# Kernel tuning notes

Measured on AMD Instinct MI355X. Metric: run time of the kernel, lower is better.

## Reference

```python
import jax, jax.numpy as jnp
import numpy as np

B, S, E, D, M, HN, NH, T, NS, OUT = 64, 196, 512, 2048, 25, 32, 8, 50, 512, 1000
HD = E // NH


def setup_inputs() -> dict:
    key = jax.random.key(0)
    ks = jax.random.split(key, 24)
    rn = lambda k, sh, sc: jax.random.normal(k, sh, jnp.float32) * sc
    iv = lambda n: 1.0 / np.sqrt(n).astype(np.float32)
    inp = {}
    inp['x'] = rn(ks[0], (B, S, E), 1.0)
    inp['Wkv'] = rn(ks[1], (E, E), iv(E)); inp['bkv'] = jnp.zeros((E,))
    inp['g_kv'] = jnp.ones((E,)); inp['b_kv'] = jnp.zeros((E,))
    inp['Wq'] = rn(ks[2], (NS, E), iv(NS)); inp['bq'] = jnp.zeros((E,))
    inp['Wqa'] = rn(ks[3], (E, E), iv(E)); inp['bqa'] = jnp.zeros((E,))
    inp['Wka'] = rn(ks[4], (E, E), iv(E)); inp['bka'] = jnp.zeros((E,))
    inp['Wva'] = rn(ks[5], (E, E), iv(E)); inp['bva'] = jnp.zeros((E,))
    inp['Wo'] = rn(ks[6], (E, E), iv(E)); inp['bo'] = jnp.zeros((E,))
    inp['Wsyn'] = rn(ks[7], (E + D, 2 * D), iv(E + D)); inp['bsyn'] = jnp.zeros((2 * D,))
    inp['g_syn'] = jnp.ones((D,)); inp['b_syn'] = jnp.zeros((D,))
    inp['w1'] = rn(ks[8], (M, 2 * HN, D), iv(M)); inp['b1'] = jnp.zeros((D, 2 * HN))
    inp['w2'] = rn(ks[9], (HN, 2, D), iv(HN)); inp['b2'] = jnp.zeros((D, 2))
    inp['start_act'] = rn(ks[10], (D,), iv(D))
    inp['start_trace'] = rn(ks[11], (D, M), iv(D + M))
    inp['decay_action'] = jax.random.uniform(ks[12], (NS,), jnp.float32)
    inp['decay_out'] = jax.random.uniform(ks[13], (NS,), jnp.float32)
    inp['Wout'] = rn(ks[14], (NS, OUT), iv(NS)); inp['bout'] = jnp.zeros((OUT,))
    inp['idx_act_l'] = jax.random.randint(ks[15], (NS,), 0, D, jnp.int32)
    inp['idx_act_r'] = jax.random.randint(ks[16], (NS,), 0, D, jnp.int32)
    inp['idx_out_l'] = jax.random.randint(ks[17], (NS,), 0, D, jnp.int32)
    inp['idx_out_r'] = jax.random.randint(ks[18], (NS,), 0, D, jnp.int32)
    return inp


def _ln(v, g, b):
    mu = v.mean(-1, keepdims=True)
    var = ((v - mu) ** 2).mean(-1, keepdims=True)
    return (v - mu) / jnp.sqrt(var + 1e-5) * g + b


def _glu(v):
    h = v.shape[-1] // 2
    return v[..., :h] * jax.nn.sigmoid(v[..., h:])


def reference(x, Wkv, bkv, g_kv, b_kv, Wq, bq, Wqa, bqa, Wka, bka, Wva, bva, Wo, bo,
              Wsyn, bsyn, g_syn, b_syn, w1, b1, w2, b2, start_act, start_trace,
              decay_action, decay_out, Wout, bout,
              idx_act_l, idx_act_r, idx_out_l, idx_out_r):
    # kv features: LazyLinear + LayerNorm (backbone='none')
    kv = _ln(x @ Wkv + bkv, g_kv, b_kv)                      # (B,S,E)
    kh = (kv @ Wka + bka).reshape(B, S, NH, HD)               # precompute K/V heads
    vh = (kv @ Wva + bva).reshape(B, S, NH, HD)
    rA = jnp.exp(-jnp.clip(decay_action, 0.0, 15.0))[None]    # (1,NS)
    rO = jnp.exp(-jnp.clip(decay_out, 0.0, 15.0))[None]
    act0 = jnp.broadcast_to(start_act[None], (B, D))
    tr0 = jnp.broadcast_to(start_trace[None], (B, D, M))
    # initial 'out' sync from start state (decay_alpha=None branch)
    aO0 = act0[:, idx_out_l] * act0[:, idx_out_r]
    bO0 = jnp.ones_like(aO0)
    aA0 = jnp.zeros((B, NS), x.dtype)
    bA0 = jnp.zeros((B, NS), x.dtype)

    def nlm(tr):  # private per-neuron deep MLPs over memory history
        h = _glu(jnp.einsum('bdm,mhd->bdh', tr, w1) + b1[None])
        o = _glu(jnp.einsum('bdh,hod->bdo', h, w2) + b2[None])
        return o[..., 0]                                      # (B,D)

    def step(carry, _):
        tr, act, aA, bA, aO, bO = carry
        pA = act[:, idx_act_l] * act[:, idx_act_r]
        aA = rA * aA + pA
        bA = rA * bA + 1.0
        syncA = aA / jnp.sqrt(bA)
        q = syncA @ Wq + bq                                   # (B,E)
        qh = (q @ Wqa + bqa).reshape(B, NH, HD)
        sc = jnp.einsum('bhd,bshd->bhs', qh, kh) / np.sqrt(HD).astype(np.float32)
        attn = jnp.einsum('bhs,bshd->bhd', jax.nn.softmax(sc, -1), vh)
        attn = attn.reshape(B, E) @ Wo + bo
        pre = jnp.concatenate([attn, act], -1)                # (B,E+D)
        s = _ln(_glu(pre @ Wsyn + bsyn), g_syn, b_syn)        # synapse MLP -> (B,D)
        tr = jnp.concatenate([tr[:, :, 1:], s[:, :, None]], -1)
        act = nlm(tr)
        pO = act[:, idx_out_l] * act[:, idx_out_r]
        aO = rO * aO + pO
        bO = rO * bO + 1.0
        syncO = aO / jnp.sqrt(bO)
        pred = syncO @ Wout + bout                            # (B,OUT)
        logp = jax.nn.log_softmax(pred, -1)
        ne = -(jnp.exp(logp) * logp).sum(-1) / np.log(OUT).astype(np.float32)
        cert = jnp.stack([ne, 1.0 - ne], -1)                  # (B,2)
        return (tr, act, aA, bA, aO, bO), (pred, cert)

    carry, (preds, certs) = jax.lax.scan(step, (tr0, act0, aA0, bA0, aO0, bO0), None, length=T)
    predictions = jnp.moveaxis(preds, 0, -1)                  # (B,OUT,T)
    certainties = jnp.moveaxis(certs, 0, -1)                  # (B,2,T)
    sync_out_final = carry[4] / jnp.sqrt(carry[5])
    return predictions, certainties, sync_out_final
```

## Files before the change

kernel.cpp:

```cpp
#include <hip/hip_runtime.h>

#define BB 64
#define SS 196
#define EE 512
#define DD 2048
#define MM 25
#define HNN 32
#define NHH 8
#define TT 50
#define NSS 512
#define OUTN 1000
#define HDD 64
#define KSYN 2560
#define NSYN 4096

#define CERT_OFF 3200000
#define SYNC_OFF 3206400

__device__ __forceinline__ float sigm(float x){ return 1.f / (1.f + expf(-x)); }
__device__ __forceinline__ int rfl(int x){ return __builtin_amdgcn_readfirstlane(x); }

template<int LAYOUT>
__global__ __launch_bounds__(256) void sgemm(
    const float* __restrict__ Ag, const float* __restrict__ Wg,
    const float* __restrict__ bias, float* __restrict__ Cg,
    int Mg, int Ng, int Kg, int ro)
{
  __shared__ float As[16][68];
  __shared__ float Bs[16][68];
  int t = threadIdx.x;
  int bm = blockIdx.x * 64, bn = blockIdx.y * 64;
  int ty = t >> 4, tx = t & 15;
  int atm = t >> 2, atk = (t & 3) * 4;
  int bkk = t >> 4, bnn = (t & 15) * 4;
  float c[4][4] = {};
  for (int k0 = 0; k0 < Kg; k0 += 16){
    float4 av = *reinterpret_cast<const float4*>(Ag + (size_t)(bm + atm) * Kg + k0 + atk);
    As[atk][atm] = av.x; As[atk + 1][atm] = av.y;
    As[atk + 2][atm] = av.z; As[atk + 3][atm] = av.w;
    float4 bv = *reinterpret_cast<const float4*>(Wg + (size_t)(k0 + bkk) * Ng + bn + bnn);
    *reinterpret_cast<float4*>(&Bs[bkk][bnn]) = bv;
    __syncthreads();
    #pragma unroll
    for (int k = 0; k < 16; k++){
      float4 a = *reinterpret_cast<const float4*>(&As[k][ty * 4]);
      float4 b = *reinterpret_cast<const float4*>(&Bs[k][tx * 4]);
      c[0][0] += a.x * b.x; c[0][1] += a.x * b.y; c[0][2] += a.x * b.z; c[0][3] += a.x * b.w;
      c[1][0] += a.y * b.x; c[1][1] += a.y * b.y; c[1][2] += a.y * b.z; c[1][3] += a.y * b.w;
      c[2][0] += a.z * b.x; c[2][1] += a.z * b.y; c[2][2] += a.z * b.z; c[2][3] += a.z * b.w;
      c[3][0] += a.w * b.x; c[3][1] += a.w * b.y; c[3][2] += a.w * b.z; c[3][3] += a.w * b.w;
    }
    __syncthreads();
  }
  #pragma unroll
  for (int j = 0; j < 4; j++){
    int col = bn + tx * 4 + j;
    float bvv = bias ? bias[col] : 0.f;
    #pragma unroll
    for (int i = 0; i < 4; i++){
      int row = bm + ty * 4 + i;
      float v = c[i][j] + bvv;
      if (LAYOUT == 0){
        Cg[(size_t)row * Ng + col] = v;
      } else {
        int tok = ro + row;
        int b = tok / SS, s = tok - b * SS;
        int h = col >> 6, dh = col & 63;
        if (LAYOUT == 1) Cg[(((size_t)b * NHH + h) * SS + s) * HDD + dh] = v;
        else             Cg[(((size_t)b * NHH + h) * HDD + dh) * SS + s] = v;
      }
    }
  }
}

__global__ __launch_bounds__(256) void ln_rows_kernel(const float* __restrict__ y,
    const float* __restrict__ g, const float* __restrict__ bb,
    float* __restrict__ outf)
{
  int r = blockIdx.x, t = threadIdx.x;
  __shared__ float red[256];
  const float* row = y + (size_t)r * EE;
  float v0 = row[t], v1 = row[t + 256];
  red[t] = v0 + v1; __syncthreads();
  for (int st = 128; st > 0; st >>= 1){ if (t < st) red[t] += red[t + st]; __syncthreads(); }
  float mean = red[0] * (1.f / EE); __syncthreads();
  float d0 = v0 - mean, d1 = v1 - mean;
  red[t] = d0 * d0 + d1 * d1; __syncthreads();
  for (int st = 128; st > 0; st >>= 1){ if (t < st) red[t] += red[t + st]; __syncthreads(); }
  float rs = 1.f / sqrtf(red[0] * (1.f / EE) + 1e-5f);
  float* orow = outf + (size_t)r * EE;
  orow[t] = d0 * rs * g[t] + bb[t];
  orow[t + 256] = d1 * rs * g[t + 256] + bb[t + 256];
}

__global__ __launch_bounds__(512) void bqq_kernel(const float* __restrict__ bq,
    const float* __restrict__ Wqa, const float* __restrict__ bqa, float* __restrict__ bqq)
{
  __shared__ float s[EE];
  int t = threadIdx.x;
  s[t] = bq[t]; __syncthreads();
  float a0 = 0, a1 = 0, a2 = 0, a3 = 0;
  #pragma unroll 8
  for (int k = 0; k < EE; k += 4){
    a0 += s[k]     * Wqa[(size_t)(k)     * EE + t];
    a1 += s[k + 1] * Wqa[(size_t)(k + 1) * EE + t];
    a2 += s[k + 2] * Wqa[(size_t)(k + 2) * EE + t];
    a3 += s[k + 3] * Wqa[(size_t)(k + 3) * EE + t];
  }
  bqq[t] = bqa[t] + ((a0 + a1) + (a2 + a3));
}

__global__ __launch_bounds__(512) void prep_decay(const float* __restrict__ dcA,
    const float* __restrict__ dcO, float* __restrict__ rA, float* __restrict__ rO)
{
  int t = threadIdx.x;
  rA[t] = expf(-fminf(fmaxf(dcA[t], 0.f), 15.f));
  rO[t] = expf(-fminf(fmaxf(dcO[t], 0.f), 15.f));
}

__global__ __launch_bounds__(256) void permute_wsyn(const float* __restrict__ Wsyn,
    float* __restrict__ W2)
{
  int k = blockIdx.x;
  const float* src = Wsyn + (size_t)k * NSYN;
  float* dst = W2 + (size_t)k * NSYN;
  for (int c = threadIdx.x; c < 2048; c += 256){
    float2 v; v.x = src[c]; v.y = src[2048 + c];
    *reinterpret_cast<float2*>(&dst[2 * c]) = v;
  }
}

__global__ __launch_bounds__(256) void init_kernel(const float* __restrict__ sa,
    const float* __restrict__ strace,
    const int* __restrict__ ol, const int* __restrict__ orr,
    float* __restrict__ act, float* __restrict__ tr,
    float* __restrict__ aA, float* __restrict__ bA,
    float* __restrict__ aO, float* __restrict__ bO,
    float* __restrict__ psum, float* __restrict__ psq)
{
  int tid = blockIdx.x * 256 + threadIdx.x;
  if (tid < 128){ psum[tid] = 0.f; psq[tid] = 0.f; }
  int b = tid >> 11, d = tid & 2047;
  act[(size_t)d * 64 + b] = sa[d];
  for (int m = 0; m < MM; m++)
    tr[((size_t)m * DD + d) * 64 + b] = strace[d * MM + m];
  if (tid < BB * NSS){
    int n = tid & (NSS - 1);
    int b2 = tid >> 9;
    aO[(size_t)b2 * NSS + n] = sa[ol[n]] * sa[orr[n]];
    bO[(size_t)b2 * NSS + n] = 1.f;
    aA[(size_t)b2 * NSS + n] = 0.f;
    bA[(size_t)b2 * NSS + n] = 0.f;
  }
}

__global__ __launch_bounds__(512) void k_front(
    const float* __restrict__ khT, const float* __restrict__ vh,
    const float* __restrict__ Wqq, const float* __restrict__ bqq,
    const float* __restrict__ Wo, const float* __restrict__ bo,
    const float* __restrict__ rA, const float* __restrict__ rO,
    const int* __restrict__ ial, const int* __restrict__ iar,
    const int* __restrict__ iol, const int* __restrict__ ior,
    float* __restrict__ aA, float* __restrict__ bA,
    float* __restrict__ aO, float* __restrict__ bO,
    const float* __restrict__ act, float* __restrict__ A,
    float* __restrict__ so_g, float* __restrict__ dout, int t)
{
  __shared__ float sm[4096];
  const int tid = threadIdx.x, b = blockIdx.x;
  const int lane = tid & 63, wv = tid >> 6;
  {
    int n = tid;
    if (t < TT){
      float pa = act[(size_t)ial[n] * 64 + b] * act[(size_t)iar[n] * 64 + b];
      float r = rA[n];
      float na = r * aA[(size_t)b * NSS + n] + pa;
      float nb = r * bA[(size_t)b * NSS + n] + 1.f;
      aA[(size_t)b * NSS + n] = na; bA[(size_t)b * NSS + n] = nb;
      sm[n] = na / sqrtf(nb);
    }
    if (t > 0){
      float po = act[(size_t)iol[n] * 64 + b] * act[(size_t)ior[n] * 64 + b];
      float r2 = rO[n];
      float na2 = r2 * aO[(size_t)b * NSS + n] + po;
      float nb2 = r2 * bO[(size_t)b * NSS + n] + 1.f;
      aO[(size_t)b * NSS + n] = na2; bO[(size_t)b * NSS + n] = nb2;
      float sv = na2 / sqrtf(nb2);
      so_g[(size_t)b * NSS + n] = sv;
      if (t == TT) dout[SYNC_OFF + (size_t)b * NSS + n] = sv;
    }
  }
  if (t >= TT) return;
  __syncthreads();
  {
    int e = tid;
    float a0 = 0, a1 = 0, a2 = 0, a3 = 0;
    #pragma unroll 8
    for (int k = 0; k < EE; k += 4){
      a0 += sm[k]     * Wqq[(size_t)(k)     * EE + e];
      a1 += sm[k + 1] * Wqq[(size_t)(k + 1) * EE + e];
      a2 += sm[k + 2] * Wqq[(size_t)(k + 2) * EE + e];
      a3 += sm[k + 3] * Wqq[(size_t)(k + 3) * EE + e];
    }
    sm[1024 + e] = bqq[e] + ((a0 + a1) + (a2 + a3));
  }
  __syncthreads();
  {
    int h = wv;
    int u = b * NHH + h;
    const float* K = khT + (size_t)u * HDD * SS;
    const float* V = vh + (size_t)u * SS * HDD;
    float c0 = 0, c1 = 0, c2 = 0, c3 = 0;
    for (int d2 = 0; d2 < HDD; d2++){
      float qd = sm[1024 + h * 64 + d2];
      const float* Kr = K + (size_t)d2 * SS;
      c0 += qd * Kr[lane];
      c1 += qd * Kr[64 + lane];
      c2 += qd * Kr[128 + lane];
      c3 += qd * Kr[192 + lane];
    }
    float s0 = c0 * 0.125f, s1 = c1 * 0.125f, s2 = c2 * 0.125f;
    float s3 = (lane < 4) ? c3 * 0.125f : -1e30f;
    float mx = fmaxf(fmaxf(s0, s1), fmaxf(s2, s3));
    #pragma unroll
    for (int off = 32; off > 0; off >>= 1)
      mx = fmaxf(mx, __shfl_xor(mx, off, 64));
    float e0 = expf(s0 - mx), e1 = expf(s1 - mx), e2 = expf(s2 - mx);
    float e3 = (lane < 4) ? expf(s3 - mx) : 0.f;
    float dn = e0 + e1 + e2 + e3;
    #pragma unroll
    for (int off = 32; off > 0; off >>= 1)
      dn += __shfl_xor(dn, off, 64);
    float* ps = sm + 1536 + h * 224;
    ps[lane] = e0; ps[64 + lane] = e1; ps[128 + lane] = e2;
    if (lane < 4) ps[192 + lane] = e3;
    float inv = 1.f / dn;
    float p0 = 0, p1 = 0, p2 = 0, p3 = 0;
    for (int s = 0; s < SS; s += 4){
      p0 += ps[s]     * V[(size_t)(s)     * 64 + lane];
      p1 += ps[s + 1] * V[(size_t)(s + 1) * 64 + lane];
      p2 += ps[s + 2] * V[(size_t)(s + 2) * 64 + lane];
      p3 += ps[s + 3] * V[(size_t)(s + 3) * 64 + lane];
    }
    sm[3328 + h * 64 + lane] = ((p0 + p1) + (p2 + p3)) * inv;
  }
  __syncthreads();
  {
    int e = tid;
    float a0 = 0, a1 = 0, a2 = 0, a3 = 0;
    #pragma unroll 8
    for (int k = 0; k < EE; k += 4){
      a0 += sm[3328 + k]     * Wo[(size_t)(k)     * EE + e];
      a1 += sm[3328 + k + 1] * Wo[(size_t)(k + 1) * EE + e];
      a2 += sm[3328 + k + 2] * Wo[(size_t)(k + 2) * EE + e];
      a3 += sm[3328 + k + 3] * Wo[(size_t)(k + 3) * EE + e];
    }
    A[(size_t)e * 64 + b] = bo[e] + ((a0 + a1) + (a2 + a3));
  }
}

__global__ __launch_bounds__(512) void k_syn2(
    const float* __restrict__ A, const float* __restrict__ W2,
    const float* __restrict__ bsyn, const float* __restrict__ Wout,
    const float* __restrict__ bout, const float* __restrict__ so_g,
    float* __restrict__ glupre, float* __restrict__ psum, float* __restrict__ psq,
    float* __restrict__ dout, int t)
{
  __shared__ float sm[8704];
  const int tid = threadIdx.x, blk = blockIdx.x;
  const int lane = tid & 63, wv = tid >> 6;
  const int par = t & 1;
  if (blk < 256){
    if (t >= TT) return;
    int c0 = blk * 8;
    int cc = 2 * c0;
    float acc[16];
    #pragma unroll
    for (int i = 0; i < 16; i++) acc[i] = 0.f;
    int kb = rfl(wv * 320);
    const float* Wp = W2 + (size_t)kb * NSYN + cc;
    const float* Ap = A + (size_t)kb * 64 + lane;
    for (int kt = 0; kt < 320; kt += 4){
      float a4[4];
      float4 w4[4][4];
      #pragma unroll
      for (int i = 0; i < 4; i++){
        a4[i] = Ap[(size_t)(kt + i) * 64];
        const float4* w = reinterpret_cast<const float4*>(Wp + (size_t)(kt + i) * NSYN);
        w4[i][0] = w[0]; w4[i][1] = w[1]; w4[i][2] = w[2]; w4[i][3] = w[3];
      }
      #pragma unroll
      for (int i = 0; i < 4; i++){
        float a = a4[i];
        acc[0]  += a * w4[i][0].x; acc[8]  += a * w4[i][0].y;
        acc[1]  += a * w4[i][0].z; acc[9]  += a * w4[i][0].w;
        acc[2]  += a * w4[i][1].x; acc[10] += a * w4[i][1].y;
        acc[3]  += a * w4[i][1].z; acc[11] += a * w4[i][1].w;
        acc[4]  += a * w4[i][2].x; acc[12] += a * w4[i][2].y;
        acc[5]  += a * w4[i][2].z; acc[13] += a * w4[i][2].w;
        acc[6]  += a * w4[i][3].x; acc[14] += a * w4[i][3].y;
        acc[7]  += a * w4[i][3].z; acc[15] += a * w4[i][3].w;
      }
    }
    #pragma unroll
    for (int i = 0; i < 16; i++) sm[wv * 1024 + i * 64 + lane] = acc[i];
    __syncthreads();
    {
      int ci = tid >> 6;
      int b = lane;
      float x0 = 0.f, x1 = 0.f;
      #pragma unroll
      for (int w = 0; w < 8; w++){
        x0 += sm[w * 1024 + ci * 64 + b];
        x1 += sm[w * 1024 + (8 + ci) * 64 + b];
      }
      x0 += bsyn[c0 + ci]; x1 += bsyn[2048 + c0 + ci];
      float u = x0 * sigm(x1);
      glupre[(size_t)(c0 + ci) * 64 + b] = u;
      sm[8192 + ci * 64 + b] = u;
    }
    __syncthreads();
    if (tid < 64){
      float s = 0.f, q = 0.f;
      #pragma unroll
      for (int c = 0; c < 8; c++){
        float uu = sm[8192 + c * 64 + tid];
        s += uu; q += uu * uu;
      }
      atomicAdd(&psum[par * 64 + tid], s);
      atomicAdd(&psq[par * 64 + tid], q);
    }
  } else {
    if (t == 0) return;
    int b = blk - 256;
    for (int k = tid; k < NSS; k += 512) sm[k] = so_g[(size_t)b * NSS + k];
    __syncthreads();
    #pragma unroll
    for (int half = 0; half < 2; half++){
      int n = tid + half * 512;
      if (n < OUTN){
        float a0 = 0, a1 = 0, a2 = 0, a3 = 0;
        #pragma unroll 8
        for (int k = 0; k < NSS; k += 4){
          a0 += sm[k]     * Wout[(size_t)(k)     * OUTN + n];
          a1 += sm[k + 1] * Wout[(size_t)(k + 1) * OUTN + n];
          a2 += sm[k + 2] * Wout[(size_t)(k + 2) * OUTN + n];
          a3 += sm[k + 3] * Wout[(size_t)(k + 3) * OUTN + n];
        }
        dout[((size_t)b * OUTN + n) * TT + (t - 1)] = bout[n] + ((a0 + a1) + (a2 + a3));
      }
    }
  }
}

__global__ __launch_bounds__(512) void k_nlm(
    const float* __restrict__ glupre, float* __restrict__ psum, float* __restrict__ psq,
    const float* __restrict__ gsyn, const float* __restrict__ bsn,
    const float* __restrict__ w1, const float* __restrict__ b1,
    const float* __restrict__ w2, const float* __restrict__ b2,
    float* __restrict__ tr, float* __restrict__ act, int t)
{
  __shared__ float sm[12800];
  const int tid = threadIdx.x, blk = blockIdx.x;
  const int lane = tid & 63, wv = tid >> 6;
  const int par = t & 1;
  if (blk == 0 && tid < 64){
    psum[(par ^ 1) * 64 + tid] = 0.f;
    psq[(par ^ 1) * 64 + tid] = 0.f;
  }
  int d0 = blk * 8;
  for (int idx = tid; idx < 1600; idx += 512){
    float4 va = *reinterpret_cast<const float4*>(w1 + (size_t)idx * DD + d0);
    float4 vb = *reinterpret_cast<const float4*>(w1 + (size_t)idx * DD + d0 + 4);
    sm[0 * 1600 + idx] = va.x; sm[1 * 1600 + idx] = va.y;
    sm[2 * 1600 + idx] = va.z; sm[3 * 1600 + idx] = va.w;
    sm[4 * 1600 + idx] = vb.x; sm[5 * 1600 + idx] = vb.y;
    sm[6 * 1600 + idx] = vb.z; sm[7 * 1600 + idx] = vb.w;
  }
  float ts = psum[par * 64 + lane];
  float tq = psq[par * 64 + lane];
  float mean = ts * (1.f / DD);
  float var = tq * (1.f / DD) - mean * mean;
  float rsv = 1.f / sqrtf(var + 1e-5f);
  __syncthreads();
  int dd = rfl(wv);
  int d = d0 + dd;
  float u = glupre[(size_t)d * 64 + lane];
  float snew = (u - mean) * rsv * gsyn[d] + bsn[d];
  int slot = t % MM;
  tr[((size_t)slot * DD + d) * 64 + lane] = snew;
  float hp[64];
  #pragma unroll
  for (int h = 0; h < 64; h++) hp[h] = b1[(size_t)d * 64 + h];
  for (int j = 0; j < MM - 1; j++){
    int js = (t + 1 + j) % MM;
    float tv = tr[((size_t)js * DD + d) * 64 + lane];
    const float* wr = &sm[dd * 1600 + j * 64];
    #pragma unroll
    for (int h4 = 0; h4 < 16; h4++){
      float4 w = *reinterpret_cast<const float4*>(&wr[h4 * 4]);
      hp[h4 * 4 + 0] += tv * w.x;
      hp[h4 * 4 + 1] += tv * w.y;
      hp[h4 * 4 + 2] += tv * w.z;
      hp[h4 * 4 + 3] += tv * w.w;
    }
  }
  {
    const float* wr = &sm[dd * 1600 + 24 * 64];
    #pragma unroll
    for (int h4 = 0; h4 < 16; h4++){
      float4 w = *reinterpret_cast<const float4*>(&wr[h4 * 4]);
      hp[h4 * 4 + 0] += snew * w.x;
      hp[h4 * 4 + 1] += snew * w.y;
      hp[h4 * 4 + 2] += snew * w.z;
      hp[h4 * 4 + 3] += snew * w.w;
    }
  }
  float o0 = b2[(size_t)d * 2], o1 = b2[(size_t)d * 2 + 1];
  #pragma unroll
  for (int h2 = 0; h2 < HNN; h2++){
    float hh = hp[h2] * sigm(hp[h2 + HNN]);
    o0 += hh * w2[((size_t)(h2 * 2)) * DD + d];
    o1 += hh * w2[((size_t)(h2 * 2 + 1)) * DD + d];
  }
  act[(size_t)d * 64 + lane] = o0 * sigm(o1);
}

__global__ __launch_bounds__(256) void cert_kernel(float* __restrict__ dout)
{
  int blk = blockIdx.x;
  int b = blk / TT, t = blk % TT;
  int tid = threadIdx.x;
  __shared__ float red[256];
  float vals[4];
  float mx = -1e30f;
  #pragma unroll
  for (int i = 0; i < 4; i++){
    int n = tid + i * 256;
    float v = (n < OUTN) ? dout[((size_t)b * OUTN + n) * TT + t] : -1e30f;
    vals[i] = v; mx = fmaxf(mx, v);
  }
  red[tid] = mx; __syncthreads();
  for (int st = 128; st > 0; st >>= 1){ if (tid < st) red[tid] = fmaxf(red[tid], red[tid + st]); __syncthreads(); }
  mx = red[0]; __syncthreads();
  float z = 0.f, s1 = 0.f;
  #pragma unroll
  for (int i = 0; i < 4; i++){
    int n = tid + i * 256;
    if (n < OUTN){
      float e = expf(vals[i] - mx);
      z += e; s1 += e * (vals[i] - mx);
    }
  }
  red[tid] = z; __syncthreads();
  for (int st = 128; st > 0; st >>= 1){ if (tid < st) red[tid] += red[tid + st]; __syncthreads(); }
  z = red[0]; __syncthreads();
  red[tid] = s1; __syncthreads();
  for (int st = 128; st > 0; st >>= 1){ if (tid < st) red[tid] += red[tid + st]; __syncthreads(); }
  s1 = red[0];
  if (tid == 0){
    float ne = (logf(z) - s1 / z) * (1.f / logf(1000.f));
    dout[CERT_OFF + ((size_t)b * 2 + 0) * TT + t] = ne;
    dout[CERT_OFF + ((size_t)b * 2 + 1) * TT + t] = 1.f - ne;
  }
}

extern "C" void kernel_launch(void* const* d_in, const int* in_sizes, int n_in,
                              void* d_out, int out_size, void* d_ws, size_t ws_size,
                              hipStream_t stream)
{
  const float* x    = (const float*)d_in[0];
  const float* Wkv  = (const float*)d_in[1];
  const float* bkv  = (const float*)d_in[2];
  const float* gkv  = (const float*)d_in[3];
  const float* bkv2 = (const float*)d_in[4];
  const float* Wq   = (const float*)d_in[5];
  const float* bq   = (const float*)d_in[6];
  const float* Wqa  = (const float*)d_in[7];
  const float* bqa  = (const float*)d_in[8];
  const float* Wka  = (const float*)d_in[9];
  const float* bka  = (const float*)d_in[10];
  const float* Wva  = (const float*)d_in[11];
  const float* bva  = (const float*)d_in[12];
  const float* Wo   = (const float*)d_in[13];
  const float* bo   = (const float*)d_in[14];
  const float* Wsyn = (const float*)d_in[15];
  const float* bsyn = (const float*)d_in[16];
  const float* gsyn = (const float*)d_in[17];
  const float* bsn  = (const float*)d_in[18];
  const float* w1   = (const float*)d_in[19];
  const float* b1   = (const float*)d_in[20];
  const float* w2   = (const float*)d_in[21];
  const float* b2   = (const float*)d_in[22];
  const float* sact = (const float*)d_in[23];
  const float* strc = (const float*)d_in[24];
  const float* dcA  = (const float*)d_in[25];
  const float* dcO  = (const float*)d_in[26];
  const float* Wout = (const float*)d_in[27];
  const float* bout = (const float*)d_in[28];
  const int* ial = (const int*)d_in[29];
  const int* iar = (const int*)d_in[30];
  const int* iol = (const int*)d_in[31];
  const int* ior = (const int*)d_in[32];

  char* ws = (char*)d_ws;
  float* khT  = (float*)(ws + 0);
  float* vh   = (float*)(ws + 25690112);
  float* B0   = (float*)(ws + 51380224);
  float* B1   = (float*)(ws + 64225280);
  float* tr    = (float*)(ws + 51380224);
  float* A     = (float*)(ws + 64487424);
  float* act   = A + 512 * 64;
  float* glupre= (float*)(ws + 65142784);
  float* aA    = (float*)(ws + 65667072);
  float* bA    = (float*)(ws + 65798144);
  float* aO    = (float*)(ws + 65929216);
  float* bO    = (float*)(ws + 66060288);
  float* so_g  = (float*)(ws + 66191360);
  float* Wqq   = (float*)(ws + 66322432);
  float* bqqb  = (float*)(ws + 67371008);
  float* rA    = (float*)(ws + 67373056);
  float* rO    = (float*)(ws + 67375104);
  float* psum  = (float*)(ws + 67377152);
  float* psq   = (float*)(ws + 67377664);
  float* W2    = (float*)(ws + 77070336);
  float* dout = (float*)d_out;

  for (int c = 0; c < 2; c++){
    const float* xc = x + (size_t)c * 6272 * EE;
    sgemm<0><<<dim3(98, 8), 256, 0, stream>>>(xc, Wkv, bkv, B0, 6272, EE, EE, 0);
    ln_rows_kernel<<<6272, 256, 0, stream>>>(B0, gkv, bkv2, B1);
    sgemm<3><<<dim3(98, 8), 256, 0, stream>>>(B1, Wka, bka, khT, 6272, EE, EE, c * 6272);
    sgemm<1><<<dim3(98, 8), 256, 0, stream>>>(B1, Wva, bva, vh, 6272, EE, EE, c * 6272);
  }
  sgemm<0><<<dim3(8, 8), 256, 0, stream>>>(Wq, Wqa, nullptr, Wqq, EE, EE, EE, 0);
  bqq_kernel<<<1, 512, 0, stream>>>(bq, Wqa, bqa, bqqb);
  permute_wsyn<<<KSYN, 256, 0, stream>>>(Wsyn, W2);
  prep_decay<<<1, 512, 0, stream>>>(dcA, dcO, rA, rO);
  init_kernel<<<512, 256, 0, stream>>>(sact, strc, iol, ior, act, tr, aA, bA, aO, bO,
                                       psum, psq);

  for (int t = 0; t < TT; t++){
    k_front<<<64, 512, 0, stream>>>(khT, vh, Wqq, bqqb, Wo, bo, rA, rO,
                                    ial, iar, iol, ior, aA, bA, aO, bO,
                                    act, A, so_g, dout, t);
    k_syn2<<<320, 512, 0, stream>>>(A, W2, bsyn, Wout, bout, so_g,
                                    glupre, psum, psq, dout, t);
    k_nlm<<<256, 512, 0, stream>>>(glupre, psum, psq, gsyn, bsn,
                                   w1, b1, w2, b2, tr, act, t);
  }
  k_front<<<64, 512, 0, stream>>>(khT, vh, Wqq, bqqb, Wo, bo, rA, rO,
                                  ial, iar, iol, ior, aA, bA, aO, bO,
                                  act, A, so_g, dout, TT);
  k_syn2<<<320, 512, 0, stream>>>(A, W2, bsyn, Wout, bout, so_g,
                                  glupre, psum, psq, dout, TT);
  cert_kernel<<<BB * TT, 256, 0, stream>>>(dout);
}
```

Baseline: 6.571 ms.

## Double k_front threads with split-K GEMVs and split attention heads

k_front now runs 1024 threads per block instead of 512. The two 512x512 GEMVs are split along K into two halves that are reduced through shared memory. Each attention head is handled by two waves, with cross-wave max and denominator reductions and split PV accumulation. This targets the latency of a kernel that launches only 64 blocks per step, at the cost of extra barriers and shared-memory reductions. Separately, the k_syn2 inner loop is unrolled to 8 rows per iteration to put more loads in flight, which raises register pressure.

```diff
diff --git a/kernel.cpp b/kernel.cpp
--- a/kernel.cpp
+++ b/kernel.cpp
@@ -154,7 +154,7 @@
   }
 }
 
-__global__ __launch_bounds__(512) void k_front(
+__global__ __launch_bounds__(1024) void k_front(
     const float* __restrict__ khT, const float* __restrict__ vh,
     const float* __restrict__ Wqq, const float* __restrict__ bqq,
     const float* __restrict__ Wo, const float* __restrict__ bo,
@@ -166,10 +166,17 @@
     const float* __restrict__ act, float* __restrict__ A,
     float* __restrict__ so_g, float* __restrict__ dout, int t)
 {
-  __shared__ float sm[4096];
+  __shared__ float sA[512];
+  __shared__ float q2[512];
+  __shared__ float ao[512];
+  __shared__ float ps[8][224];
+  __shared__ float red[1024];
+  __shared__ float mxred[8][2];
+  __shared__ float dnred[8][2];
+  __shared__ float paov[8][2][64];
   const int tid = threadIdx.x, b = blockIdx.x;
-  const int lane = tid & 63, wv = tid >> 6;
-  {
+  const int lane = tid & 63;
+  if (tid < 512){
     int n = tid;
     if (t < TT){
       float pa = act[(size_t)ial[n] * 64 + b] * act[(size_t)iar[n] * 64 + b];
@@ -177,8 +184,10 @@
       float na = r * aA[(size_t)b * NSS + n] + pa;
       float nb = r * bA[(size_t)b * NSS + n] + 1.f;
       aA[(size_t)b * NSS + n] = na; bA[(size_t)b * NSS + n] = nb;
-      sm[n] = na / sqrtf(nb);
-    }
+      sA[n] = na / sqrtf(nb);
+    }
+  } else {
+    int n = tid - 512;
     if (t > 0){
       float po = act[(size_t)iol[n] * 64 + b] * act[(size_t)ior[n] * 64 + b];
       float r2 = rO[n];
@@ -193,70 +202,86 @@
   if (t >= TT) return;
   __syncthreads();
   {
-    int e = tid;
+    int e = tid & 511, ks = tid >> 9;
+    int k0 = ks * 256;
     float a0 = 0, a1 = 0, a2 = 0, a3 = 0;
     #pragma unroll 8
-    for (int k = 0; k < EE; k += 4){
-      a0 += sm[k]     * Wqq[(size_t)(k)     * EE + e];
-      a1 += sm[k + 1] * Wqq[(size_t)(k + 1) * EE + e];
-      a2 += sm[k + 2] * Wqq[(size_t)(k + 2) * EE + e];
-      a3 += sm[k + 3] * Wqq[(size_t)(k + 3) * EE + e];
-    }
-    sm[1024 + e] = bqq[e] + ((a0 + a1) + (a2 + a3));
-  }
+    for (int k = k0; k < k0 + 256; k += 4){
+      a0 += sA[k]     * Wqq[(size_t)(k)     * EE + e];
+      a1 += sA[k + 1] * Wqq[(size_t)(k + 1) * EE + e];
+      a2 += sA[k + 2] * Wqq[(size_t)(k + 2) * EE + e];
+      a3 += sA[k + 3] * Wqq[(size_t)(k + 3) * EE + e];
+    }
+    red[ks * 512 + e] = (a0 + a1) + (a2 + a3);
+  }
+  __syncthreads();
+  if (tid < 512) q2[tid] = bqq[tid] + red[tid] + red[512 + tid];
   __syncthreads();
   {
-    int h = wv;
+    int wv = tid >> 6;
+    int h = wv >> 1, half = wv & 1;
     int u = b * NHH + h;
     const float* K = khT + (size_t)u * HDD * SS;
     const float* V = vh + (size_t)u * SS * HDD;
-    float c0 = 0, c1 = 0, c2 = 0, c3 = 0;
+    float c0 = 0, c1 = 0;
+    int o0 = half * 128, o1 = half * 128 + 64;
     for (int d2 = 0; d2 < HDD; d2++){
-      float qd = sm[1024 + h * 64 + d2];
+      float qd = q2[h * 64 + d2];
       const float* Kr = K + (size_t)d2 * SS;
-      c0 += qd * Kr[lane];
-      c1 += qd * Kr[64 + lane];
-      c2 += qd * Kr[128 + lane];
-      c3 += qd * Kr[192 + lane];
-    }
-    float s0 = c0 * 0.125f, s1 = c1 * 0.125f, s2 = c2 * 0.125f;
-    float s3 = (lane < 4) ? c3 * 0.125f : -1e30f;
-    float mx = fmaxf(fmaxf(s0, s1), fmaxf(s2, s3));
+      c0 += qd * Kr[o0 + lane];
+      c1 += qd * Kr[o1 + lane];
+    }
+    float s0 = c0 * 0.125f;
+    bool v1 = (half == 0) || (lane < 4);
+    float s1 = v1 ? c1 * 0.125f : -1e30f;
+    float mx = fmaxf(s0, s1);
     #pragma unroll
     for (int off = 32; off > 0; off >>= 1)
       mx = fmaxf(mx, __shfl_xor(mx, off, 64));
-    float e0 = expf(s0 - mx), e1 = expf(s1 - mx), e2 = expf(s2 - mx);
-    float e3 = (lane < 4) ? expf(s3 - mx) : 0.f;
-    float dn = e0 + e1 + e2 + e3;
+    if (lane == 0) mxred[h][half] = mx;
+    __syncthreads();
+    mx = fmaxf(mxred[h][0], mxred[h][1]);
+    float e0 = expf(s0 - mx);
+    float e1 = v1 ? expf(s1 - mx) : 0.f;
+    ps[h][o0 + lane] = e0;
+    if (v1) ps[h][o1 + lane] = e1;
+    float dn = e0 + e1;
     #pragma unroll
     for (int off = 32; off > 0; off >>= 1)
       dn += __shfl_xor(dn, off, 64);
-    float* ps = sm + 1536 + h * 224;
-    ps[lane] = e0; ps[64 + lane] = e1; ps[128 + lane] = e2;
-    if (lane < 4) ps[192 + lane] = e3;
-    float inv = 1.f / dn;
+    if (lane == 0) dnred[h][half] = dn;
+    __syncthreads();
+    float inv = 1.f / (dnred[h][0] + dnred[h][1]);
+    int sbeg = half ? 96 : 0;
+    int send = half ? 196 : 96;
     float p0 = 0, p1 = 0, p2 = 0, p3 = 0;
-    for (int s = 0; s < SS; s += 4){
-      p0 += ps[s]     * V[(size_t)(s)     * 64 + lane];
-      p1 += ps[s + 1] * V[(size_t)(s + 1) * 64 + lane];
-      p2 += ps[s + 2] * V[(size_t)(s + 2) * 64 + lane];
-      p3 += ps[s + 3] * V[(size_t)(s + 3) * 64 + lane];
-    }
-    sm[3328 + h * 64 + lane] = ((p0 + p1) + (p2 + p3)) * inv;
+    for (int s = sbeg; s < send; s += 4){
+      p0 += ps[h][s]     * V[(size_t)(s)     * 64 + lane];
+      p1 += ps[h][s + 1] * V[(size_t)(s + 1) * 64 + lane];
+      p2 += ps[h][s + 2] * V[(size_t)(s + 2) * 64 + lane];
+      p3 += ps[h][s + 3] * V[(size_t)(s + 3) * 64 + lane];
+    }
+    paov[h][half][lane] = (p0 + p1) + (p2 + p3);
+    __syncthreads();
+    if (half == 0)
+      ao[h * 64 + lane] = (paov[h][0][lane] + paov[h][1][lane]) * inv;
   }
   __syncthreads();
   {
-    int e = tid;
+    int e = tid & 511, ks = tid >> 9;
+    int k0 = ks * 256;
     float a0 = 0, a1 = 0, a2 = 0, a3 = 0;
     #pragma unroll 8
-    for (int k = 0; k < EE; k += 4){
-      a0 += sm[3328 + k]     * Wo[(size_t)(k)     * EE + e];
-      a1 += sm[3328 + k + 1] * Wo[(size_t)(k + 1) * EE + e];
-      a2 += sm[3328 + k + 2] * Wo[(size_t)(k + 2) * EE + e];
-      a3 += sm[3328 + k + 3] * Wo[(size_t)(k + 3) * EE + e];
-    }
-    A[(size_t)e * 64 + b] = bo[e] + ((a0 + a1) + (a2 + a3));
-  }
+    for (int k = k0; k < k0 + 256; k += 4){
+      a0 += ao[k]     * Wo[(size_t)(k)     * EE + e];
+      a1 += ao[k + 1] * Wo[(size_t)(k + 1) * EE + e];
+      a2 += ao[k + 2] * Wo[(size_t)(k + 2) * EE + e];
+      a3 += ao[k + 3] * Wo[(size_t)(k + 3) * EE + e];
+    }
+    red[ks * 512 + e] = (a0 + a1) + (a2 + a3);
+  }
+  __syncthreads();
+  if (tid < 512) A[(size_t)tid * 64 + b] = bo[tid] + red[tid] + red[512 + tid];
 }
 
 __global__ __launch_bounds__(512) void k_syn2(
@@ -280,26 +305,26 @@
     int kb = rfl(wv * 320);
     const float* Wp = W2 + (size_t)kb * NSYN + cc;
     const float* Ap = A + (size_t)kb * 64 + lane;
-    for (int kt = 0; kt < 320; kt += 4){
-      float a4[4];
-      float4 w4[4][4];
+    for (int kt = 0; kt < 320; kt += 8){
+      float a8[8];
+      float4 w8[8][4];
       #pragma unroll
-      for (int i = 0; i < 4; i++){
-        a4[i] = Ap[(size_t)(kt + i) * 64];
+      for (int i = 0; i < 8; i++){
+        a8[i] = Ap[(size_t)(kt + i) * 64];
         const float4* w = reinterpret_cast<const float4*>(Wp + (size_t)(kt + i) * NSYN);
-        w4[i][0] = w[0]; w4[i][1] = w[1]; w4[i][2] = w[2]; w4[i][3] = w[3];
+        w8[i][0] = w[0]; w8[i][1] = w[1]; w8[i][2] = w[2]; w8[i][3] = w[3];
       }
       #pragma unroll
-      for (int i = 0; i < 4; i++){
-        float a = a4[i];
-        acc[0]  += a * w4[i][0].x; acc[8]  += a * w4[i][0].y;
-        acc[1]  += a * w4[i][0].z; acc[9]  += a * w4[i][0].w;
-        acc[2]  += a * w4[i][1].x; acc[10] += a * w4[i][1].y;
-        acc[3]  += a * w4[i][1].z; acc[11] += a * w4[i][1].w;
-        acc[4]  += a * w4[i][2].x; acc[12] += a * w4[i][2].y;
-        acc[5]  += a * w4[i][2].z; acc[13] += a * w4[i][2].w;
-        acc[6]  += a * w4[i][3].x; acc[14] += a * w4[i][3].y;
-        acc[7]  += a * w4[i][3].z; acc[15] += a * w4[i][3].w;
+      for (int i = 0; i < 8; i++){
+        float a = a8[i];
+        acc[0]  += a * w8[i][0].x; acc[8]  += a * w8[i][0].y;
+        acc[1]  += a * w8[i][0].z; acc[9]  += a * w8[i][0].w;
+        acc[2]  += a * w8[i][1].x; acc[10] += a * w8[i][1].y;
+        acc[3]  += a * w8[i][1].z; acc[11] += a * w8[i][1].w;
+        acc[4]  += a * w8[i][2].x; acc[12] += a * w8[i][2].y;
+        acc[5]  += a * w8[i][2].z; acc[13] += a * w8[i][2].w;
+        acc[6]  += a * w8[i][3].x; acc[14] += a * w8[i][3].y;
+        acc[7]  += a * w8[i][3].z; acc[15] += a * w8[i][3].w;
       }
     }
     #pragma unroll
@@ -541,17 +566,17 @@
                                        psum, psq);
 
   for (int t = 0; t < TT; t++){
-    k_front<<<64, 512, 0, stream>>>(khT, vh, Wqq, bqqb, Wo, bo, rA, rO,
-                                    ial, iar, iol, ior, aA, bA, aO, bO,
-                                    act, A, so_g, dout, t);
+    k_front<<<64, 1024, 0, stream>>>(khT, vh, Wqq, bqqb, Wo, bo, rA, rO,
+                                     ial, iar, iol, ior, aA, bA, aO, bO,
+                                     act, A, so_g, dout, t);
     k_syn2<<<320, 512, 0, stream>>>(A, W2, bsyn, Wout, bout, so_g,
                                     glupre, psum, psq, dout, t);
     k_nlm<<<256, 512, 0, stream>>>(glupre, psum, psq, gsyn, bsn,
                                    w1, b1, w2, b2, tr, act, t);
   }
-  k_front<<<64, 512, 0, stream>>>(khT, vh, Wqq, bqqb, Wo, bo, rA, rO,
-                                  ial, iar, iol, ior, aA, bA, aO, bO,
-                                  act, A, so_g, dout, TT);
+  k_front<<<64, 1024, 0, stream>>>(khT, vh, Wqq, bqqb, Wo, bo, rA, rO,
+                                   ial, iar, iol, ior, aA, bA, aO, bO,
+                                   act, A, so_g, dout, TT);
   k_syn2<<<320, 512, 0, stream>>>(A, W2, bsyn, Wout, bout, so_g,
                                   glupre, psum, psq, dout, TT);
   cert_kernel<<<BB * TT, 256, 0, stream>>>(dout);
```

New measurement: 6.842 ms. +4.1%, slower.
